# Kernel optimization log

Hardware: AMD Instinct MI355X
Metric: run time of the kernel (lower is better)

## Reference

```python
import jax, jax.numpy as jnp
import numpy as np

NUM_HEAD = 16
DIM_HEAD = 64
IN_DIM = NUM_HEAD * DIM_HEAD
SLEN = 1024
BSZ = 32
LN_EPS = 1e-5


def setup_inputs() -> dict:
    key = jax.random.key(0)
    ks = jax.random.split(key, 8)
    std = 1.0 / np.sqrt(DIM_HEAD)
    std_q = 0.01 / np.sqrt(DIM_HEAD)
    h = jax.random.normal(ks[0], (SLEN, BSZ, IN_DIM), dtype=jnp.float32)
    W_y = std * jax.random.normal(ks[1], (1, NUM_HEAD, DIM_HEAD, DIM_HEAD), dtype=jnp.float32)
    W_q = std_q * jax.random.normal(ks[2], (1, NUM_HEAD, DIM_HEAD, DIM_HEAD), dtype=jnp.float32)
    W_k = std * jax.random.normal(ks[3], (1, NUM_HEAD, DIM_HEAD, DIM_HEAD), dtype=jnp.float32)
    w_b = -1.0 + std * jax.random.normal(ks[4], (1, NUM_HEAD, DIM_HEAD, 4), dtype=jnp.float32)
    out_w = (1.0 / np.sqrt(IN_DIM)) * jax.random.normal(ks[5], (IN_DIM, IN_DIM), dtype=jnp.float32)  # (out, in), no bias
    ln_g = jnp.ones((IN_DIM,), dtype=jnp.float32)
    ln_b = jnp.zeros((IN_DIM,), dtype=jnp.float32)
    return {"h": h, "W_y": W_y, "W_q": W_q, "W_k": W_k, "w_b": w_b,
            "out_w": out_w, "ln_g": ln_g, "ln_b": ln_b}


def _layer_norm(x, g, b):
    mu = jnp.mean(x, axis=-1, keepdims=True)
    var = jnp.mean(jnp.square(x - mu), axis=-1, keepdims=True)
    return (x - mu) * jax.lax.rsqrt(var + LN_EPS) * g + b


def _srwm_forward(h, W_y, W_q, W_k, w_b, out_w, ln_g, ln_b):
    slen, bsz, in_dim = h.shape
    H, D = W_y.shape[1], W_y.shape[2]
    x = h.reshape(slen, bsz, H, D)  # (T,B,H,D) -- scan over leading T

    Wy0 = jnp.broadcast_to(W_y, (bsz, H, D, D))
    Wq0 = jnp.broadcast_to(W_q, (bsz, H, D, D))
    Wk0 = jnp.broadcast_to(W_k, (bsz, H, D, D))
    wb0 = jnp.broadcast_to(w_b, (bsz, H, D, 4))

    def step(carry, x_t):
        Wy, Wq, Wk, wb = carry  # (B,H,D,D) / (B,H,D,4)
        y = jnp.einsum('bhod,bhd->bho', Wy, x_t)
        q = jax.nn.softmax(jnp.einsum('bhod,bhd->bho', Wq, x_t), axis=-1)
        k = jax.nn.softmax(jnp.einsum('bhod,bhd->bho', Wk, x_t), axis=-1)
        beta = jax.nn.sigmoid(jnp.einsum('bhdk,bhd->bhk', wb, x_t))  # (B,H,4)
        # old values (keyed by k) and new target values (keyed by q)
        yk = jnp.einsum('bhod,bhd->bho', Wy, k); yq = jnp.einsum('bhod,bhd->bho', Wy, q)
        qk = jnp.einsum('bhod,bhd->bho', Wq, k); qq = jnp.einsum('bhod,bhd->bho', Wq, q)
        kk = jnp.einsum('bhod,bhd->bho', Wk, k); kq = jnp.einsum('bhod,bhd->bho', Wk, q)
        bk = jnp.einsum('bhdk,bhd->bhk', wb, k); bq = jnp.einsum('bhdk,bhd->bhk', wb, q)
        # delta-rule rank-1 self-modification, per-submatrix learned rate
        Wy = Wy + beta[..., 0, None, None] * ((yq - yk)[..., :, None] * k[..., None, :])
        Wq = Wq + beta[..., 1, None, None] * ((qq - qk)[..., :, None] * k[..., None, :])
        Wk = Wk + beta[..., 2, None, None] * ((kq - kk)[..., :, None] * k[..., None, :])
        wb = wb + beta[..., 3, None, None] * (k[..., :, None] * (bq - bk)[..., None, :])
        out_t = jax.nn.softmax(y, axis=-1)  # v0 applies softmax on y
        return (Wy, Wq, Wk, wb), out_t

    _, ys = jax.lax.scan(step, (Wy0, Wq0, Wk0, wb0), x)  # ys: (T,B,H,D)
    out = ys.reshape(slen, bsz, H * D)
    out = out @ out_w.T  # out_linear, no bias
    out = _layer_norm(h, ln_g, ln_b) + out  # use_ln + use_res
    return out


def reference(h, W_y, W_q, W_k, w_b, out_w, ln_g, ln_b):
    return _srwm_forward(h, W_y, W_q, W_k, w_b, out_w, ln_g, ln_b)
```

## Files before the change

### kernel.cpp

```cpp
#include <hip/hip_runtime.h>
#include <hip/hip_bf16.h>

#define SLEN 1024
#define BSZ 32
#define NHEAD 16
#define DHEAD 64
#define INDIM 1024

typedef __attribute__((ext_vector_type(8))) __bf16 bf16x8;
typedef __attribute__((ext_vector_type(4))) float f32x4;
typedef __attribute__((ext_vector_type(2))) float f32x2;

#if __has_builtin(__builtin_elementwise_fma)
__device__ __forceinline__ f32x2 pk_fma(f32x2 a, f32x2 b, f32x2 c) {
  return __builtin_elementwise_fma(a, b, c);
}
#else
__device__ __forceinline__ f32x2 pk_fma(f32x2 a, f32x2 b, f32x2 c) {
  f32x2 r; r.x = fmaf(a.x, b.x, c.x); r.y = fmaf(a.y, b.y, c.y); return r;
}
#endif

template <int C>
__device__ __forceinline__ float dppmov(float v) {
  return __int_as_float(__builtin_amdgcn_update_dpp(
      __float_as_int(v), __float_as_int(v), C, 0xF, 0xF, false));
}
__device__ __forceinline__ float wred_sum_u(float v) {
  v += dppmov<0x111>(v);
  v += dppmov<0x112>(v);
  v += dppmov<0x114>(v);
  v += dppmov<0x118>(v);
  v += dppmov<0x142>(v);
  v += dppmov<0x143>(v);
  return __int_as_float(__builtin_amdgcn_readlane(__float_as_int(v), 63));
}
__device__ __forceinline__ float wred_max_u(float v) {
  v = fmaxf(v, dppmov<0x111>(v));
  v = fmaxf(v, dppmov<0x112>(v));
  v = fmaxf(v, dppmov<0x114>(v));
  v = fmaxf(v, dppmov<0x118>(v));
  v = fmaxf(v, dppmov<0x142>(v));
  v = fmaxf(v, dppmov<0x143>(v));
  return __int_as_float(__builtin_amdgcn_readlane(__float_as_int(v), 63));
}

__global__ __launch_bounds__(256, 2) void srwm_scan(
    const float* __restrict__ h,
    const float* __restrict__ Wy0, const float* __restrict__ Wq0,
    const float* __restrict__ Wk0, const float* __restrict__ wb0,
    __hip_bfloat16* __restrict__ ys)
{
  const int p  = blockIdx.x;
  const int b  = p >> 4;
  const int hd = p & 15;
  const int tid = threadIdx.x;
  const int w = tid >> 6, l = tid & 63;

  __shared__ float sx[2][64];
  __shared__ float sq[2][64];
  __shared__ float sk[2][64];
  __shared__ float sbeta[2][4];
  __shared__ __hip_bfloat16 ysbuf[8][64];

  f32x2 wrow[32];
  f32x2 kr[32];
  float sc_pend = 0.f;
  float xnext = 0.f;
  float cshift = 0.f;

  if (w < 3) {
    const float* base = (w == 0) ? Wy0 : (w == 1) ? Wq0 : Wk0;
    const float4* s4 = (const float4*)(base + (size_t)(hd * DHEAD + l) * DHEAD);
#pragma unroll
    for (int c = 0; c < 16; ++c) {
      const float4 v = s4[c];
      wrow[2 * c + 0] = f32x2{v.x, v.y};
      wrow[2 * c + 1] = f32x2{v.z, v.w};
    }
#pragma unroll
    for (int c = 0; c < 32; ++c) kr[c] = (f32x2)(0.f);
    if (w == 2) sk[1][l] = 0.f;
  } else {
    const float4 v = *(const float4*)(wb0 + (size_t)(hd * DHEAD + l) * 4);
    wrow[0] = f32x2{v.x, v.y};
    wrow[1] = f32x2{v.z, v.w};
    sx[0][l] = h[(size_t)b * INDIM + hd * DHEAD + l];
    xnext = h[(size_t)BSZ * INDIM + (size_t)b * INDIM + hd * DHEAD + l];
  }
  __syncthreads();

  const size_t xstride = (size_t)BSZ * INDIM;
  const float* xsrc = h + (size_t)b * INDIM + hd * DHEAD + l;
  __hip_bfloat16* ybase = ys + (size_t)b * INDIM + hd * DHEAD;

#pragma unroll 2
  for (int t = 0; t < SLEN; ++t) {
    const int cur = t & 1, nxt = cur ^ 1, prev = nxt;
    if (w < 3) {
      const float* xb = sx[cur];
      f32x2 a0 = (f32x2)(0.f), a1 = (f32x2)(0.f);
      f32x2 a2 = (f32x2)(0.f), a3 = (f32x2)(0.f);
#pragma unroll
      for (int c = 0; c < 8; ++c) {
        const float4 x0 = *(const float4*)(xb + 8 * c);
        const float4 x1 = *(const float4*)(xb + 8 * c + 4);
        a0 = pk_fma(wrow[4 * c + 0], f32x2{x0.x, x0.y}, a0);
        a1 = pk_fma(wrow[4 * c + 1], f32x2{x0.z, x0.w}, a1);
        a2 = pk_fma(wrow[4 * c + 2], f32x2{x1.x, x1.y}, a2);
        a3 = pk_fma(wrow[4 * c + 3], f32x2{x1.z, x1.w}, a3);
      }
      const f32x2 as = (a0 + a1) + (a2 + a3);
      const float rl = sk[prev][l] * xb[l];
      const float r  = wred_sum_u(rl);
      const float a  = (as.x + as.y) + sc_pend * r;
      const float e = __expf(a - cshift);
      const float mnew = wred_max_u(a);
      const float s = wred_sum_u(e);
      const float sm = e * __builtin_amdgcn_rcpf(s);
      cshift = mnew;
      if (w == 0) {
        ysbuf[t & 7][l] = __float2bfloat16(sm);
      } else if (w == 1) {
        sq[cur][l] = sm;
      } else {
        sk[cur][l] = sm;
      }
      const f32x2 spv = (f32x2)(sc_pend);
#pragma unroll
      for (int c = 0; c < 32; ++c) wrow[c] = pk_fma(spv, kr[c], wrow[c]);
    } else {
      sx[nxt][l] = xnext;
      const float xd = sx[cur][l];
      const float z0 = wred_sum_u(wrow[0].x * xd);
      const float z1 = wred_sum_u(wrow[0].y * xd);
      const float z2 = wred_sum_u(wrow[1].x * xd);
      const float z3 = wred_sum_u(wrow[1].y * xd);
      if (l == 0) {
        sbeta[cur][0] = __builtin_amdgcn_rcpf(1.f + __expf(-z0));
        sbeta[cur][1] = __builtin_amdgcn_rcpf(1.f + __expf(-z1));
        sbeta[cur][2] = __builtin_amdgcn_rcpf(1.f + __expf(-z2));
        sbeta[cur][3] = __builtin_amdgcn_rcpf(1.f + __expf(-z3));
      }
    }
    __syncthreads();
    if (w < 3) {
      if (w == 0 && (t & 7) == 7) {
        const uint4 v = ((const uint4*)ysbuf)[l];
        const int t0 = t - 7 + (l >> 3);
        *(uint4*)(ybase + (size_t)t0 * xstride + (l & 7) * 8) = v;
      }
      const float* qb = sq[cur];
      const float* kb = sk[cur];
      const float beta = sbeta[cur][w];
      f32x2 d0 = (f32x2)(0.f), d1 = (f32x2)(0.f);
      f32x2 d2 = (f32x2)(0.f), d3 = (f32x2)(0.f);
#pragma unroll
      for (int c = 0; c < 8; ++c) {
        const float4 q0 = *(const float4*)(qb + 8 * c);
        const float4 q1 = *(const float4*)(qb + 8 * c + 4);
        const float4 k0 = *(const float4*)(kb + 8 * c);
        const float4 k1 = *(const float4*)(kb + 8 * c + 4);
        const f32x2 ka = f32x2{k0.x, k0.y}, kb2 = f32x2{k0.z, k0.w};
        const f32x2 kc = f32x2{k1.x, k1.y}, kd = f32x2{k1.z, k1.w};
        kr[4 * c + 0] = ka; kr[4 * c + 1] = kb2;
        kr[4 * c + 2] = kc; kr[4 * c + 3] = kd;
        d0 = pk_fma(wrow[4 * c + 0], f32x2{q0.x, q0.y} - ka,  d0);
        d1 = pk_fma(wrow[4 * c + 1], f32x2{q0.z, q0.w} - kb2, d1);
        d2 = pk_fma(wrow[4 * c + 2], f32x2{q1.x, q1.y} - kc,  d2);
        d3 = pk_fma(wrow[4 * c + 3], f32x2{q1.z, q1.w} - kd,  d3);
      }
      const f32x2 ds = (d0 + d1) + (d2 + d3);
      sc_pend = beta * (ds.x + ds.y);
    } else {
      const int tload = (t + 2 < SLEN) ? (t + 2) : (SLEN - 1);
      xnext = xsrc[(size_t)tload * xstride];
      const float qd = sq[cur][l], kd = sk[cur][l];
      const float dd = qd - kd;
      const float z0 = wred_sum_u(wrow[0].x * dd);
      const float z1 = wred_sum_u(wrow[0].y * dd);
      const float z2 = wred_sum_u(wrow[1].x * dd);
      const float z3 = wred_sum_u(wrow[1].y * dd);
      const float s3 = sbeta[cur][3] * kd;
      wrow[0].x = fmaf(s3, z0, wrow[0].x);
      wrow[0].y = fmaf(s3, z1, wrow[0].y);
      wrow[1].x = fmaf(s3, z2, wrow[1].x);
      wrow[1].y = fmaf(s3, z3, wrow[1].y);
    }
  }
}

__global__ __launch_bounds__(256) void ln_stats(
    const float* __restrict__ h, float2* __restrict__ stats)
{
  const int row = blockIdx.x * 4 + (threadIdx.x >> 6);
  const int l = threadIdx.x & 63;
  const float4* hp = (const float4*)(h + (size_t)row * INDIM);
  float s = 0.f, s2 = 0.f;
#pragma unroll
  for (int c = 0; c < 4; ++c) {
    const float4 v = hp[c * 64 + l];
    s  += v.x + v.y + v.z + v.w;
    s2 += v.x * v.x + v.y * v.y + v.z * v.z + v.w * v.w;
  }
  s  = wred_sum_u(s);
  s2 = wred_sum_u(s2);
  if (l == 0) {
    const float mu  = s * (1.f / INDIM);
    const float var = s2 * (1.f / INDIM) - mu * mu;
    stats[row] = make_float2(mu, rsqrtf(var + 1e-5f));
  }
}

__global__ void cvt_bf16(const float* __restrict__ src,
                         __hip_bfloat16* __restrict__ dst, int n)
{
  const int i = blockIdx.x * blockDim.x + threadIdx.x;
  if (i < n) dst[i] = __float2bfloat16(src[i]);
}

__global__ __launch_bounds__(256) void gemm_ln(
    const __hip_bfloat16* __restrict__ A,
    const __hip_bfloat16* __restrict__ Bw,
    const float* __restrict__ h,
    const float2* __restrict__ stats,
    const float* __restrict__ g,
    const float* __restrict__ bvec,
    float* __restrict__ out)
{
  const int K = INDIM;
  __shared__ __align__(16) __hip_bfloat16 As[128 * 32];
  __shared__ __align__(16) __hip_bfloat16 Bs[128 * 32];
  const int tid = threadIdx.x, w = tid >> 6, l = tid & 63;
  const int wm = w >> 1, wn = w & 1;
  const int m0 = blockIdx.x * 128, n0 = blockIdx.y * 128;

  f32x4 acc[4][4];
#pragma unroll
  for (int i = 0; i < 4; ++i)
#pragma unroll
    for (int j = 0; j < 4; ++j) acc[i][j] = (f32x4)(0.f);

  const int mr = tid >> 2;
  const int kc = (tid & 3) * 8;

  for (int k0 = 0; k0 < K; k0 += 32) {
    const uint4 va0 = *(const uint4*)(A  + (size_t)(m0 + mr)      * K + k0 + kc);
    const uint4 va1 = *(const uint4*)(A  + (size_t)(m0 + mr + 64) * K + k0 + kc);
    const uint4 vb0 = *(const uint4*)(Bw + (size_t)(n0 + mr)      * K + k0 + kc);
    const uint4 vb1 = *(const uint4*)(Bw + (size_t)(n0 + mr + 64) * K + k0 + kc);
    *(uint4*)((char*)As + (size_t)tid * 16)         = va0;
    *(uint4*)((char*)As + (size_t)(tid + 256) * 16) = va1;
    *(uint4*)((char*)Bs + (size_t)tid * 16)         = vb0;
    *(uint4*)((char*)Bs + (size_t)(tid + 256) * 16) = vb1;
    __syncthreads();

    bf16x8 af[4], bfr[4];
    const int koff = (l >> 4) * 16;
#pragma unroll
    for (int i = 0; i < 4; ++i) {
      af[i]  = *(const bf16x8*)((const char*)As +
                 (size_t)(wm * 64 + i * 16 + (l & 15)) * 64 + koff);
      bfr[i] = *(const bf16x8*)((const char*)Bs +
                 (size_t)(wn * 64 + i * 16 + (l & 15)) * 64 + koff);
    }
#pragma unroll
    for (int i = 0; i < 4; ++i)
#pragma unroll
      for (int j = 0; j < 4; ++j)
        acc[i][j] = __builtin_amdgcn_mfma_f32_16x16x32_bf16(
            af[i], bfr[j], acc[i][j], 0, 0, 0);
    __syncthreads();
  }

  float gv[4], bv[4];
  int cols[4];
#pragma unroll
  for (int j = 0; j < 4; ++j) {
    const int col = n0 + wn * 64 + j * 16 + (l & 15);
    cols[j] = col; gv[j] = g[col]; bv[j] = bvec[col];
  }
#pragma unroll
  for (int i = 0; i < 4; ++i) {
#pragma unroll
    for (int r = 0; r < 4; ++r) {
      const int row = m0 + wm * 64 + i * 16 + (l >> 4) * 4 + r;
      const float2 st = stats[row];
      const float* hrow = h + (size_t)row * INDIM;
      float* orow = out + (size_t)row * INDIM;
#pragma unroll
      for (int j = 0; j < 4; ++j) {
        const float lnv = (hrow[cols[j]] - st.x) * st.y * gv[j] + bv[j];
        orow[cols[j]] = acc[i][j][r] + lnv;
      }
    }
  }
}

extern "C" void kernel_launch(void* const* d_in, const int* in_sizes, int n_in,
                              void* d_out, int out_size, void* d_ws, size_t ws_size,
                              hipStream_t stream)
{
  const float* h    = (const float*)d_in[0];
  const float* Wy   = (const float*)d_in[1];
  const float* Wq   = (const float*)d_in[2];
  const float* Wk   = (const float*)d_in[3];
  const float* wb   = (const float*)d_in[4];
  const float* outw = (const float*)d_in[5];
  const float* lng  = (const float*)d_in[6];
  const float* lnb  = (const float*)d_in[7];
  float* out = (float*)d_out;

  char* ws = (char*)d_ws;
  __hip_bfloat16* ys  = (__hip_bfloat16*)ws;
  __hip_bfloat16* wbf = (__hip_bfloat16*)(ws + 67108864);
  float2*       stats = (float2*)(ws + 67108864 + 2097152);

  cvt_bf16 <<<4096, 256, 0, stream>>>(outw, wbf, INDIM * INDIM);
  ln_stats <<<8192, 256, 0, stream>>>(h, stats);
  srwm_scan<<<512,  256, 0, stream>>>(h, Wy, Wq, Wk, wb, ys);
  gemm_ln  <<<dim3(256, 8), 256, 0, stream>>>(ys, wbf, h, stats, lng, lnb, out);
}
```

Measured before the change: 1.625 ms.

## Apply rank-1 update eagerly, store q/k in fp16 LDS, load x per-thread from global

```diff
diff --git a/kernel.cpp b/kernel.cpp
--- a/kernel.cpp
+++ b/kernel.cpp
@@ -10,6 +10,7 @@
 typedef __attribute__((ext_vector_type(8))) __bf16 bf16x8;
 typedef __attribute__((ext_vector_type(4))) float f32x4;
 typedef __attribute__((ext_vector_type(2))) float f32x2;
+typedef __attribute__((ext_vector_type(8))) _Float16 f16x8;
 
 #if __has_builtin(__builtin_elementwise_fma)
 __device__ __forceinline__ f32x2 pk_fma(f32x2 a, f32x2 b, f32x2 c) {
@@ -57,17 +58,18 @@
   const int tid = threadIdx.x;
   const int w = tid >> 6, l = tid & 63;
 
-  __shared__ float sx[2][64];
-  __shared__ float sq[2][64];
-  __shared__ float sk[2][64];
+  __shared__ __align__(16) _Float16 sq16[2][64];
+  __shared__ __align__(16) _Float16 sk16[2][64];
   __shared__ float sbeta[2][4];
-  __shared__ __hip_bfloat16 ysbuf[8][64];
+  __shared__ __align__(16) __hip_bfloat16 ysbuf[8][64];
 
   f32x2 wrow[32];
-  f32x2 kr[32];
-  float sc_pend = 0.f;
-  float xnext = 0.f;
+  float4 xp[16];
   float cshift = 0.f;
+  float xcur = 0.f, xnxt = 0.f;
+
+  const size_t xstride = (size_t)BSZ * INDIM;
+  const float* xrow0 = h + (size_t)b * INDIM + hd * DHEAD;
 
   if (w < 3) {
     const float* base = (w == 0) ? Wy0 : (w == 1) ? Wq0 : Wk0;
@@ -78,42 +80,36 @@
       wrow[2 * c + 0] = f32x2{v.x, v.y};
       wrow[2 * c + 1] = f32x2{v.z, v.w};
     }
-#pragma unroll
-    for (int c = 0; c < 32; ++c) kr[c] = (f32x2)(0.f);
-    if (w == 2) sk[1][l] = 0.f;
+    const float4* x4 = (const float4*)xrow0;
+#pragma unroll
+    for (int i = 0; i < 16; ++i) xp[i] = x4[i];
   } else {
     const float4 v = *(const float4*)(wb0 + (size_t)(hd * DHEAD + l) * 4);
     wrow[0] = f32x2{v.x, v.y};
     wrow[1] = f32x2{v.z, v.w};
-    sx[0][l] = h[(size_t)b * INDIM + hd * DHEAD + l];
-    xnext = h[(size_t)BSZ * INDIM + (size_t)b * INDIM + hd * DHEAD + l];
+    xcur = xrow0[l];
+    xnxt = xrow0[xstride + l];
   }
   __syncthreads();
 
-  const size_t xstride = (size_t)BSZ * INDIM;
-  const float* xsrc = h + (size_t)b * INDIM + hd * DHEAD + l;
   __hip_bfloat16* ybase = ys + (size_t)b * INDIM + hd * DHEAD;
 
 #pragma unroll 2
   for (int t = 0; t < SLEN; ++t) {
-    const int cur = t & 1, nxt = cur ^ 1, prev = nxt;
+    const int cur = t & 1;
     if (w < 3) {
-      const float* xb = sx[cur];
       f32x2 a0 = (f32x2)(0.f), a1 = (f32x2)(0.f);
       f32x2 a2 = (f32x2)(0.f), a3 = (f32x2)(0.f);
 #pragma unroll
       for (int c = 0; c < 8; ++c) {
-        const float4 x0 = *(const float4*)(xb + 8 * c);
-        const float4 x1 = *(const float4*)(xb + 8 * c + 4);
+        const float4 x0 = xp[2 * c], x1 = xp[2 * c + 1];
         a0 = pk_fma(wrow[4 * c + 0], f32x2{x0.x, x0.y}, a0);
         a1 = pk_fma(wrow[4 * c + 1], f32x2{x0.z, x0.w}, a1);
         a2 = pk_fma(wrow[4 * c + 2], f32x2{x1.x, x1.y}, a2);
         a3 = pk_fma(wrow[4 * c + 3], f32x2{x1.z, x1.w}, a3);
       }
       const f32x2 as = (a0 + a1) + (a2 + a3);
-      const float rl = sk[prev][l] * xb[l];
-      const float r  = wred_sum_u(rl);
-      const float a  = (as.x + as.y) + sc_pend * r;
+      const float a = as.x + as.y;
       const float e = __expf(a - cshift);
       const float mnew = wred_max_u(a);
       const float s = wred_sum_u(e);
@@ -122,16 +118,12 @@
       if (w == 0) {
         ysbuf[t & 7][l] = __float2bfloat16(sm);
       } else if (w == 1) {
-        sq[cur][l] = sm;
+        sq16[cur][l] = (_Float16)sm;
       } else {
-        sk[cur][l] = sm;
-      }
-      const f32x2 spv = (f32x2)(sc_pend);
-#pragma unroll
-      for (int c = 0; c < 32; ++c) wrow[c] = pk_fma(spv, kr[c], wrow[c]);
+        sk16[cur][l] = (_Float16)sm;
+      }
     } else {
-      sx[nxt][l] = xnext;
-      const float xd = sx[cur][l];
+      const float xd = xcur;
       const float z0 = wred_sum_u(wrow[0].x * xd);
       const float z1 = wred_sum_u(wrow[0].y * xd);
       const float z2 = wred_sum_u(wrow[1].x * xd);
@@ -150,32 +142,47 @@
         const int t0 = t - 7 + (l >> 3);
         *(uint4*)(ybase + (size_t)t0 * xstride + (l & 7) * 8) = v;
       }
-      const float* qb = sq[cur];
-      const float* kb = sk[cur];
+      {
+        const int tn = (t + 1 < SLEN) ? (t + 1) : (SLEN - 1);
+        const float4* xn4 = (const float4*)(xrow0 + (size_t)tn * xstride);
+#pragma unroll
+        for (int i = 0; i < 16; ++i) xp[i] = xn4[i];
+      }
+      const f16x8* qv = (const f16x8*)sq16[cur];
+      const f16x8* kv = (const f16x8*)sk16[cur];
+      f16x8 kk[8], qk[8];
+#pragma unroll
+      for (int c = 0; c < 8; ++c) { kk[c] = kv[c]; qk[c] = qv[c] - kk[c]; }
       const float beta = sbeta[cur][w];
-      f32x2 d0 = (f32x2)(0.f), d1 = (f32x2)(0.f);
-      f32x2 d2 = (f32x2)(0.f), d3 = (f32x2)(0.f);
+      float d0 = 0.f, d1 = 0.f, d2 = 0.f, d3 = 0.f;
 #pragma unroll
       for (int c = 0; c < 8; ++c) {
-        const float4 q0 = *(const float4*)(qb + 8 * c);
-        const float4 q1 = *(const float4*)(qb + 8 * c + 4);
-        const float4 k0 = *(const float4*)(kb + 8 * c);
-        const float4 k1 = *(const float4*)(kb + 8 * c + 4);
-        const f32x2 ka = f32x2{k0.x, k0.y}, kb2 = f32x2{k0.z, k0.w};
-        const f32x2 kc = f32x2{k1.x, k1.y}, kd = f32x2{k1.z, k1.w};
-        kr[4 * c + 0] = ka; kr[4 * c + 1] = kb2;
-        kr[4 * c + 2] = kc; kr[4 * c + 3] = kd;
-        d0 = pk_fma(wrow[4 * c + 0], f32x2{q0.x, q0.y} - ka,  d0);
-        d1 = pk_fma(wrow[4 * c + 1], f32x2{q0.z, q0.w} - kb2, d1);
-        d2 = pk_fma(wrow[4 * c + 2], f32x2{q1.x, q1.y} - kc,  d2);
-        d3 = pk_fma(wrow[4 * c + 3], f32x2{q1.z, q1.w} - kd,  d3);
-      }
-      const f32x2 ds = (d0 + d1) + (d2 + d3);
-      sc_pend = beta * (ds.x + ds.y);
+        d0 = fmaf((float)qk[c][0], wrow[4 * c + 0].x, d0);
+        d1 = fmaf((float)qk[c][1], wrow[4 * c + 0].y, d1);
+        d2 = fmaf((float)qk[c][2], wrow[4 * c + 1].x, d2);
+        d3 = fmaf((float)qk[c][3], wrow[4 * c + 1].y, d3);
+        d0 = fmaf((float)qk[c][4], wrow[4 * c + 2].x, d0);
+        d1 = fmaf((float)qk[c][5], wrow[4 * c + 2].y, d1);
+        d2 = fmaf((float)qk[c][6], wrow[4 * c + 3].x, d2);
+        d3 = fmaf((float)qk[c][7], wrow[4 * c + 3].y, d3);
+      }
+      const float sc = beta * ((d0 + d1) + (d2 + d3));
+#pragma unroll
+      for (int c = 0; c < 8; ++c) {
+        wrow[4 * c + 0].x = fmaf((float)kk[c][0], sc, wrow[4 * c + 0].x);
+        wrow[4 * c + 0].y = fmaf((float)kk[c][1], sc, wrow[4 * c + 0].y);
+        wrow[4 * c + 1].x = fmaf((float)kk[c][2], sc, wrow[4 * c + 1].x);
+        wrow[4 * c + 1].y = fmaf((float)kk[c][3], sc, wrow[4 * c + 1].y);
+        wrow[4 * c + 2].x = fmaf((float)kk[c][4], sc, wrow[4 * c + 2].x);
+        wrow[4 * c + 2].y = fmaf((float)kk[c][5], sc, wrow[4 * c + 2].y);
+        wrow[4 * c + 3].x = fmaf((float)kk[c][6], sc, wrow[4 * c + 3].x);
+        wrow[4 * c + 3].y = fmaf((float)kk[c][7], sc, wrow[4 * c + 3].y);
+      }
     } else {
-      const int tload = (t + 2 < SLEN) ? (t + 2) : (SLEN - 1);
-      xnext = xsrc[(size_t)tload * xstride];
-      const float qd = sq[cur][l], kd = sk[cur][l];
+      xcur = xnxt;
+      const int tl = (t + 2 < SLEN) ? (t + 2) : (SLEN - 1);
+      xnxt = xrow0[(size_t)tl * xstride + l];
+      const float qd = (float)sq16[cur][l], kd = (float)sk16[cur][l];
       const float dd = qd - kd;
       const float z0 = wred_sum_u(wrow[0].x * dd);
       const float z1 = wred_sum_u(wrow[0].y * dd);
```

Result: slower. 2.200 ms (+35.4%).
